# Kernel tuning notes

Hardware: AMD Instinct MI355X
Metric: run time of the kernel (lower is better)

Reference implementation:

```python
import jax, jax.numpy as jnp
import numpy as np

ALPHA = 0.2   # LeakyReLU negative slope (init arg alpha)
H = 256       # hidden_dim
U = 1024      # user pairs -> 2U user nodes
M = 64        # UAV nodes
D = 2 * U     # uniform out-degree per UAV (edges sorted by source)
N = 2 * U + M
E = M * D


def _lstm_dir(x, w_ih, w_hh, b):
    # x: [T, B, I] -> outputs [T, B, Hc]; b = b_ih + b_hh (they only ever add)
    Hc = w_hh.shape[1]
    B = x.shape[1]
    def step(carry, xt):
        h, c = carry
        g = xt @ w_ih.T + h @ w_hh.T + b          # [B, 4*Hc], gate order i,f,g,o
        i, f, gg, o = jnp.split(g, 4, axis=-1)
        c = jax.nn.sigmoid(f) * c + jax.nn.sigmoid(i) * jnp.tanh(gg)
        h = jax.nn.sigmoid(o) * jnp.tanh(c)
        return (h, c), h
    h0 = jnp.zeros((B, Hc), x.dtype)
    _, hs = jax.lax.scan(step, (h0, h0), x)
    return hs


def _bilstm(x, wih, whh, b):
    # wih: [2, 4Hc, I]; whh: [2, 4Hc, Hc]; b: [2, 4Hc]; dir 0 = fwd, 1 = reverse
    fwd = _lstm_dir(x, wih[0], whh[0], b[0])
    rev = _lstm_dir(x[::-1], wih[1], whh[1], b[1])[::-1]
    return jnp.concatenate([fwd, rev], axis=-1)   # [T, B, 2*Hc]


def _mlp2(h, w1, b1, w2, b2):
    h = jax.nn.relu(h @ w1.T + b1)
    return jax.nn.relu(h @ w2.T + b2)


def _forward(x, edge_index, users_num,
             ul_wih, ul_whh, ul_b, uav_lin_w, uav_lin_b,
             msg_w1, msg_b1, msg_w2, msg_b2,
             wq_w, wq_b, wr_w, wr_b, att_w, att_b,
             upd_w1, upd_b1, upd_w2, upd_b2,
             uavl_wih, uavl_whh, uavl_b, lin2_w, lin2_b):
    Un = users_num
    n = x.shape[0]
    m = n - 2 * Un
    # ---- users bidirectional LSTM over the pair (seq_len=2, batch=U) ----
    seq = jnp.stack([x[:Un], x[Un:2 * Un]], axis=0)        # [2, U, 2]
    users = _bilstm(seq, ul_wih, ul_whh, ul_b)             # [2, U, H]
    users = jnp.concatenate([users[0], users[1]], axis=0)  # [2U, H]
    uavs = x[2 * Un:] @ uav_lin_w.T + uav_lin_b            # [M, H]
    h = jnp.concatenate([users, uavs], axis=0)             # [N, H]
    # ---- message passing (flow target_to_source: i=src, aggregate at src) ----
    src, tgt = edge_index[0], edge_index[1]
    xi = h[src]                                            # [E, H]
    xj = h[tgt]                                            # [E, H]
    msg = _mlp2(jnp.concatenate([xi, xj], axis=1), msg_w1, msg_b1, msg_w2, msg_b2)  # [E, H]
    q = xi @ wq_w.T + wq_b
    r = msg @ wr_w.T + wr_b
    a = jax.nn.leaky_relu(jnp.concatenate([q, r], axis=1) @ att_w.T + att_b, ALPHA)  # [E,1]
    # segment softmax: edges sorted by source, uniform degree -> reshape [M, D]
    a = jax.nn.softmax(a.reshape(m, -1), axis=1).reshape(-1, 1)
    # ---- scatter-mean aggregate over source index ----
    agg = jax.ops.segment_sum(a * msg, src, num_segments=n)          # [N, H]
    cnt = jax.ops.segment_sum(jnp.ones((src.shape[0],), x.dtype), src, num_segments=n)
    agg = agg / jnp.maximum(cnt, 1.0)[:, None]
    # ---- update ----
    h2 = _mlp2(jnp.concatenate([agg, h], axis=1), upd_w1, upd_b1, upd_w2, upd_b2)  # [N, H]
    uav_seq = h2[2 * Un:][:, None, :]                      # [M, 1, H]
    uav_out = _bilstm(uav_seq, uavl_wih, uavl_whh, uavl_b)[:, 0, :]  # [M, H]
    out = jnp.concatenate([h2[:2 * Un], uav_out], axis=0)
    return jax.nn.sigmoid(out @ lin2_w.T + lin2_b)         # [N, 2]


def setup_inputs():
    key = jax.random.key(0)
    ks = iter(jax.random.split(key, 32))
    p = lambda *s: jax.random.normal(next(ks), s, jnp.float32) * 0.05
    Hc = H // 2
    x = jax.random.uniform(next(ks), (N, 2), jnp.float32)
    src = jnp.repeat(2 * U + jnp.arange(M), D)
    tgt = jnp.tile(jnp.arange(2 * U), M)
    edge_index = jnp.stack([src, tgt]).astype(jnp.int32)
    return dict(
        x=x, edge_index=edge_index, users_num=U,
        ul_wih=p(2, 4 * Hc, 2), ul_whh=p(2, 4 * Hc, Hc), ul_b=p(2, 4 * Hc),
        uav_lin_w=p(H, 2), uav_lin_b=p(H),
        msg_w1=p(H, 2 * H), msg_b1=p(H), msg_w2=p(H, H), msg_b2=p(H),
        wq_w=p(H, H), wq_b=p(H), wr_w=p(H, H), wr_b=p(H),
        att_w=p(1, 2 * H), att_b=p(1),
        upd_w1=p(H, 2 * H), upd_b1=p(H), upd_w2=p(H, H), upd_b2=p(H),
        uavl_wih=p(2, 4 * Hc, H), uavl_whh=p(2, 4 * Hc, Hc), uavl_b=p(2, 4 * Hc),
        lin2_w=p(2, H), lin2_b=p(2),
    )


def reference(x, edge_index, users_num,
              ul_wih, ul_whh, ul_b, uav_lin_w, uav_lin_b,
              msg_w1, msg_b1, msg_w2, msg_b2,
              wq_w, wq_b, wr_w, wr_b, att_w, att_b,
              upd_w1, upd_b1, upd_w2, upd_b2,
              uavl_wih, uavl_whh, uavl_b, lin2_w, lin2_b):
    return _forward(x, edge_index, users_num,
                    ul_wih, ul_whh, ul_b, uav_lin_w, uav_lin_b,
                    msg_w1, msg_b1, msg_w2, msg_b2,
                    wq_w, wq_b, wr_w, wr_b, att_w, att_b,
                    upd_w1, upd_b1, upd_w2, upd_b2,
                    uavl_wih, uavl_whh, uavl_b, lin2_w, lin2_b)
```

## Files before the change

kernel.cpp:

```cpp
#include <hip/hip_runtime.h>
#include <hip/hip_bf16.h>
#include <hip/hip_fp16.h>
#include <math.h>

#define UQ   1024
#define NUQ  2048
#define MQ   64
#define NN   2112
#define HD   256

typedef __attribute__((ext_vector_type(4))) float f32x4;
typedef __attribute__((ext_vector_type(8))) __bf16 bf16x8;
typedef __attribute__((ext_vector_type(8))) _Float16 f16x8;

#define OFF_HB    0u
#define OFF_HUF   65536u
#define OFF_PUBF  1146880u
#define OFF_PB    2195456u
#define OFF_SPR   2260992u
#define OFF_ATT   2261248u
#define OFF_WHHT  2263552u
#define OFF_WIHT  2787840u
#define OFF_W1F   3836416u
#define OFF_W2F   4098560u
#define OFF_UW1F  4229632u
#define OFF_UW2F  4491776u
#define OFF_CREC  4622848u
#define OFF_H2U   5155328u

__device__ __forceinline__ float sigm(float v) { return 1.f / (1.f + expf(-v)); }

__device__ __forceinline__ int huf_idx(int row, int k) {
  return (((row >> 6) * 8 + (k >> 5)) * 4 + ((row >> 4) & 3)) * 512 +
         (((k >> 3) & 3) * 16 + (row & 15)) * 8 + (k & 7);
}

__device__ __forceinline__ void gl16(const void* g, void* l) {
  __builtin_amdgcn_global_load_lds((const __attribute__((address_space(1))) void*)g,
                                   (__attribute__((address_space(3))) void*)l, 16, 0, 0);
}

__device__ void tile_transpose_perm(const float* __restrict__ in, int in_ld,
                                    float* __restrict__ out, int out_ld,
                                    int k0, int c0) {
  __shared__ float ldt[64][68];
  const int t = threadIdx.x;
  {
    const int ci = t >> 2, kq = t & 3;
    const int c = c0 + ci;
    const int row = (c & 3) * 128 + (c >> 2);
    const float* src = in + row * in_ld + k0 + kq * 16;
#pragma unroll
    for (int e = 0; e < 4; ++e)
      *(f32x4*)&ldt[ci][kq * 16 + e * 4] = *(const f32x4*)(src + e * 4);
  }
  __syncthreads();
  {
    const int kk = t >> 2, cq = t & 3;
    float* dst = out + (k0 + kk) * out_ld + c0 + cq * 16;
#pragma unroll
    for (int e4 = 0; e4 < 4; ++e4) {
      f32x4 v;
#pragma unroll
      for (int j = 0; j < 4; ++j) v[j] = ldt[cq * 16 + e4 * 4 + j][kk];
      *(f32x4*)(dst + e4 * 4) = v;
    }
  }
}

template<int K, typename T>
__device__ void frag_cast16(const float* __restrict__ W, int j0, T* __restrict__ frag) {
  __shared__ float ldc[16][K + 4];
  const int t = threadIdx.x;
  {
    const int jr = t >> 4, kq = t & 15;
    const float* src = W + (j0 + jr) * K + kq * (K / 16);
#pragma unroll
    for (int e = 0; e < K / 64; ++e)
      *(f32x4*)&ldc[jr][kq * (K / 16) + e * 4] = *(const f32x4*)(src + e * 4);
  }
  __syncthreads();
  const int f = j0 >> 4;
  constexpr int nks = K >> 5;
  constexpr int thr_per_ks = 256 / nks;
  constexpr int q_per_thr = 512 / thr_per_ks;
  const int ks = t / thr_per_ks;
  const int q0 = (t % thr_per_ks) * q_per_thr;
#pragma unroll
  for (int h = 0; h < q_per_thr / 8; ++h) {
    T v[8];
#pragma unroll
    for (int e = 0; e < 8; ++e) {
      int q = q0 + h * 8 + e;
      int lane = q >> 3;
      v[e] = (T)ldc[lane & 15][ks * 32 + (lane >> 4) * 8 + (q & 7)];
    }
    *(ulong2*)(frag + (ks * 16 + f) * 512 + q0 + h * 8) = *(ulong2*)v;
  }
}

__global__ __launch_bounds__(256) void k0_prep(
    const float* __restrict__ ul_whh, const float* __restrict__ uavl_wih,
    const float* __restrict__ msg_w1, const float* __restrict__ msg_w2,
    const float* __restrict__ upd_w1, const float* __restrict__ upd_w2,
    const float* __restrict__ att_w,  const float* __restrict__ att_b,
    const float* __restrict__ wq_w,   const float* __restrict__ wq_b,
    const float* __restrict__ wr_w,   const float* __restrict__ wr_b,
    char* __restrict__ ws)
{
  const int b = blockIdx.x, t = threadIdx.x;
  if (b < 32) {
    const int dir = b >> 4, tile = b & 15;
    tile_transpose_perm(ul_whh + dir * 65536, 128,
                        (float*)(ws + OFF_WHHT) + dir * 65536, 512,
                        (tile >> 3) * 64, (tile & 7) * 64);
  } else if (b < 96) {
    const int b2 = b - 32, dir = b2 >> 5, tile = b2 & 31;
    tile_transpose_perm(uavl_wih + dir * 131072, 256,
                        (float*)(ws + OFF_WIHT) + dir * 131072, 512,
                        (tile >> 3) * 64, (tile & 7) * 64);
  } else if (b < 112) {
    frag_cast16<256, _Float16>(msg_w2, (b - 96) * 16, (_Float16*)(ws + OFF_W2F));
  } else if (b < 128) {
    frag_cast16<512, __bf16>(msg_w1, (b - 112) * 16, (__bf16*)(ws + OFF_W1F));
  } else if (b < 144) {
    frag_cast16<512, __bf16>(upd_w1, (b - 128) * 16, (__bf16*)(ws + OFF_UW1F));
  } else if (b < 160) {
    frag_cast16<256, __bf16>(upd_w2, (b - 144) * 16, (__bf16*)(ws + OFF_UW2F));
  } else {
    float* wqa = (float*)(ws + OFF_ATT);
    float* vv  = wqa + 256;
    float* c0  = wqa + 512;
    float sa = 0.f, sr = 0.f;
    for (int j = 0; j < 256; ++j) {
      sa += att_w[j]       * wq_w[j * 256 + t];
      sr += att_w[256 + j] * wr_w[j * 256 + t];
    }
    wqa[t] = sa; vv[t] = sr;
    __shared__ float red[256];
    red[t] = att_w[t] * wq_b[t] + att_w[256 + t] * wr_b[t];
    __syncthreads();
    for (int s = 128; s > 0; s >>= 1) { if (t < s) red[t] += red[t + s]; __syncthreads(); }
    if (t == 0) c0[0] = red[0] + att_b[0];
  }
}

__global__ __launch_bounds__(256) void k1_embed(
    const float* __restrict__ x, const float* __restrict__ ul_wih,
    const float* __restrict__ ul_b, const float* __restrict__ uav_lin_w,
    const float* __restrict__ uav_lin_b, char* __restrict__ ws)
{
  __bf16* huf = (__bf16*)(ws + OFF_HUF);
  const int b = blockIdx.x, tid = threadIdx.x;
  if (b < 256) {
    const float* whhT = (const float*)(ws + OFF_WHHT);
    const int dir = tid >> 7, hc = tid & 127;
    const int u0 = b * 4;
    float wx[4], wy[4], bb[4];
#pragma unroll
    for (int g = 0; g < 4; ++g) {
      int row = g * 128 + hc;
      wx[g] = ul_wih[dir * 1024 + row * 2 + 0];
      wy[g] = ul_wih[dir * 1024 + row * 2 + 1];
      bb[g] = ul_b[dir * 512 + row];
    }
    __shared__ float h1s[2][128][4];
    __shared__ float hout[8][260];
    float c1[4], h1v[4], in1x[4], in1y[4];
#pragma unroll
    for (int uu = 0; uu < 4; ++uu) {
      int u = u0 + uu;
      float ax = x[u * 2], ay = x[u * 2 + 1];
      float bx = x[(UQ + u) * 2], by = x[(UQ + u) * 2 + 1];
      float i0x = dir ? bx : ax, i0y = dir ? by : ay;
      in1x[uu] = dir ? ax : bx; in1y[uu] = dir ? ay : by;
      float gv[4];
#pragma unroll
      for (int g = 0; g < 4; ++g) gv[g] = wx[g] * i0x + wy[g] * i0y + bb[g];
      float ii = sigm(gv[0]), gg = tanhf(gv[2]), oo = sigm(gv[3]);
      c1[uu] = ii * gg;
      h1v[uu] = oo * tanhf(c1[uu]);
      h1s[dir][hc][uu] = h1v[uu];
    }
    __syncthreads();
    float acc[4][4];
#pragma unroll
    for (int uu = 0; uu < 4; ++uu)
#pragma unroll
      for (int g = 0; g < 4; ++g) acc[uu][g] = wx[g] * in1x[uu] + wy[g] * in1y[uu] + bb[g];
#pragma unroll 4
    for (int k = 0; k < 128; ++k) {
      f32x4 hv  = *(const f32x4*)&h1s[dir][k][0];
      f32x4 wv4 = *(const f32x4*)(whhT + dir * 65536 + k * 512 + hc * 4);
#pragma unroll
      for (int uu = 0; uu < 4; ++uu)
#pragma unroll
        for (int g = 0; g < 4; ++g) acc[uu][g] += hv[uu] * wv4[g];
    }
    const int col = dir * 128 + hc;
#pragma unroll
    for (int uu = 0; uu < 4; ++uu) {
      float ii = sigm(acc[uu][0]), ff = sigm(acc[uu][1]);
      float gg = tanhf(acc[uu][2]), oo = sigm(acc[uu][3]);
      float c2 = ff * c1[uu] + ii * gg;
      float h2v = oo * tanhf(c2);
      float va = dir ? h2v : h1v[uu];
      float vb = dir ? h1v[uu] : h2v;
      hout[uu][col] = va;
      hout[4 + uu][col] = vb;
    }
    __syncthreads();
    {
      const int lr = tid >> 5, c = tid & 31;
      bf16x8 v;
#pragma unroll
      for (int e = 0; e < 8; ++e) v[e] = (__bf16)hout[lr][c * 8 + e];
      const int node = (lr < 4) ? (u0 + lr) : (UQ + u0 + lr - 4);
      *(bf16x8*)(huf + huf_idx(node, c * 8)) = v;
    }
  } else {
    float* hb = (float*)(ws + OFF_HB);
    const int j = tid;
    const int mb = (b - 256) * 16;
    for (int m = mb; m < mb + 16; ++m) {
      float xa = x[(NUQ + m) * 2], xb = x[(NUQ + m) * 2 + 1];
      float val = xa * uav_lin_w[j * 2] + xb * uav_lin_w[j * 2 + 1] + uav_lin_b[j];
      hb[m * 256 + j] = val;
      huf[huf_idx(NUQ + m, j)] = (__bf16)val;
    }
  }
}

template<int G, int NKS>
__device__ __forceinline__ void frag_gemm_acc_g(const __bf16* __restrict__ Abase, int g0,
                                                const __bf16* __restrict__ Bbase,
                                                f32x4 acc[G][4]) {
  const int lane = threadIdx.x & 63;
  const int cg = threadIdx.x >> 6;
  for (int ks = 0; ks < NKS; ++ks) {
    bf16x8 Af[G], Bf[4];
#pragma unroll
    for (int g = 0; g < G; ++g)
      Af[g] = *(const bf16x8*)(Abase + ((ks * 4 + g0 + g) * 64 + lane) * 8);
#pragma unroll
    for (int f = 0; f < 4; ++f)
      Bf[f] = *(const bf16x8*)(Bbase + ((ks * 16 + cg * 4 + f) * 64 + lane) * 8);
#pragma unroll
    for (int g = 0; g < G; ++g)
#pragma unroll
      for (int f = 0; f < 4; ++f)
        acc[g][f] = __builtin_amdgcn_mfma_f32_16x16x32_bf16(Af[g], Bf[f], acc[g][f], 0, 0, 0);
  }
}

__global__ __launch_bounds__(256) void k2_proj(const float* __restrict__ msg_b1,
                                               char* __restrict__ ws)
{
  const __bf16* huf = (const __bf16*)(ws + OFF_HUF);
  const __bf16* w1f = (const __bf16*)(ws + OFF_W1F);
  const int b = blockIdx.x;
  const int tid = threadIdx.x;
  const int lane = tid & 63, cg = tid >> 6;
  const int cl = lane & 15, g16 = lane >> 4;
  if (b < 64) {
    f32x4 acc[2][4] = {};
    frag_gemm_acc_g<2, 8>(huf + (b >> 1) * 16384, (b & 1) * 2, w1f + 65536, acc);
    __shared__ float ldt[32][264];
#pragma unroll
    for (int g = 0; g < 2; ++g)
#pragma unroll
      for (int f = 0; f < 4; ++f)
#pragma unroll
        for (int r = 0; r < 4; ++r)
          ldt[g * 16 + g16 * 4 + r][cg * 64 + f * 16 + cl] = acc[g][f][r];
    __syncthreads();
    _Float16* pubf = (_Float16*)(ws + OFF_PUBF);
    const int c2 = b >> 3, r16base = (b & 7) * 2;
#pragma unroll
    for (int p = 0; p < 4; ++p) {
      const int region = p * 4 + (tid >> 6);
      const int ks = region >> 1, r16l = region & 1;
      const int row15 = tid & 15, kg = (tid >> 4) & 3;
      const int row = r16l * 16 + row15;
      f16x8 v;
#pragma unroll
      for (int j = 0; j < 8; ++j) v[j] = (_Float16)ldt[row][ks * 32 + kg * 8 + j];
      const int dst = ((c2 * 8 + ks) * 16 + (r16base + r16l)) * 512 + (kg * 16 + row15) * 8;
      *(f16x8*)(pubf + dst) = v;
    }
  } else if (b == 64) {
    f32x4 acc[4][4] = {};
    frag_gemm_acc_g<4, 8>(huf + 32 * 16384, 0, w1f, acc);
    _Float16* pb = (_Float16*)(ws + OFF_PB);
#pragma unroll
    for (int g = 0; g < 4; ++g)
#pragma unroll
      for (int f = 0; f < 4; ++f)
#pragma unroll
        for (int r = 0; r < 4; ++r) {
          int row = g * 16 + g16 * 4 + r;
          int col = cg * 64 + f * 16 + cl;
          pb[row * 256 + col] = (_Float16)(acc[g][f][r] + msg_b1[col]);
        }
  } else {
    const float* hb  = (const float*)(ws + OFF_HB);
    const float* wqa = (const float*)(ws + OFF_ATT);
    const float* c0  = wqa + 512;
    float* spr = (float*)(ws + OFF_SPR);
    if (tid < 64) {
      float s = 0.f;
      for (int k = 0; k < 256; ++k) s += hb[tid * 256 + k] * wqa[k];
      spr[tid] = s + c0[0];
    }
  }
}

__global__ __launch_bounds__(1024, 2) void k3_edge(const float* __restrict__ msg_b2,
                                                   char* __restrict__ ws)
{
  const char*     PUBF = (const char*)(ws + OFF_PUBF);
  const _Float16* PB   = (const _Float16*)(ws + OFF_PB);
  const float*    spr  = (const float*)(ws + OFF_SPR);
  const float*    vv   = (const float*)(ws + OFF_ATT) + 256;
  const char*     W2F  = (const char*)(ws + OFF_W2F);
  float* crec = (float*)(ws + OFF_CREC);

  __shared__ __align__(16) char bufA[2][16384];
  __shared__ __align__(16) char bufB[2][16384];
  __shared__ float plds[16][64];
  __shared__ float redmax[16], wds[16];
  __shared__ float wvs[4][256];

  const int m = blockIdx.x >> 3, ch = blockIdx.x & 7;
  const int tid = threadIdx.x, wave = tid >> 6, lane = tid & 63;
  const int cl = lane & 15, g16 = lane >> 4;
  const int rg = wave >> 2, cg = wave & 3;
  const int rot = (m + ch) & 7;
  const float sm = spr[m];
  const char* Asrc = PUBF + ch * 131072;
  const _Float16* pbm = PB + m * 256;
  const int bq = ((tid >> 4) & 3) * 8;

  auto repack = [](f16x8 raw, f16x8 pb8) -> f16x8 {
    f16x8 s = raw + pb8;
#pragma unroll
    for (int r = 0; r < 8; ++r) s[r] = s[r] > (_Float16)0 ? s[r] : (_Float16)0;
    return s;
  };

  {
    f16x8 raw = *(const f16x8*)(Asrc + rot * 16384 + tid * 16);
    gl16(W2F + rot * 16384 + tid * 16, &bufB[0][tid * 16]);
    f16x8 pb8 = *(const f16x8*)(pbm + rot * 32 + bq);
    *(f16x8*)(&bufA[0][tid * 16]) = repack(raw, pb8);
  }
  __syncthreads();

  f32x4 acc[4][4] = {};
  for (int i = 0; i < 8; ++i) {
    const int cur = i & 1;
    f16x8 arn{};
    f16x8 pn{};
    if (i < 7) {
      const int ksn = (i + 1 + rot) & 7;
      arn = *(const f16x8*)(Asrc + ksn * 16384 + tid * 16);
      gl16(W2F + ksn * 16384 + tid * 16, &bufB[cur ^ 1][tid * 16]);
      pn = *(const f16x8*)(pbm + ksn * 32 + bq);
    }
    f16x8 Af[4], Bf[4];
#pragma unroll
    for (int g = 0; g < 4; ++g)
      Af[g] = *(const f16x8*)(&bufA[cur][((rg * 4 + g) * 64 + lane) * 16]);
#pragma unroll
    for (int f = 0; f < 4; ++f)
      Bf[f] = *(const f16x8*)(&bufB[cur][((cg * 4 + f) * 64 + lane) * 16]);
    __builtin_amdgcn_s_setprio(1);
#pragma unroll
    for (int g = 0; g < 4; ++g)
#pragma unroll
      for (int f = 0; f < 4; ++f)
        acc[g][f] = __builtin_amdgcn_mfma_f32_16x16x32_f16(Af[g], Bf[f], acc[g][f], 0, 0, 0);
    __builtin_amdgcn_s_setprio(0);
    if (i < 7) {
      *(f16x8*)(&bufA[cur ^ 1][tid * 16]) = repack(arn, pn);
    }
    __syncthreads();
  }

  float p[4][4] = {};
#pragma unroll
  for (int f = 0; f < 4; ++f) {
    const int j = cg * 64 + f * 16 + cl;
    const float b2j = msg_b2[j], vj = vv[j];
#pragma unroll
    for (int g = 0; g < 4; ++g)
#pragma unroll
      for (int r = 0; r < 4; ++r) {
        float mv = fmaxf(acc[g][f][r] + b2j, 0.f);
        acc[g][f][r] = mv;
        p[g][r] += mv * vj;
      }
  }
#pragma unroll
  for (int mask = 1; mask < 16; mask <<= 1)
#pragma unroll
    for (int g = 0; g < 4; ++g)
#pragma unroll
      for (int r = 0; r < 4; ++r) p[g][r] += __shfl_xor(p[g][r], mask);
  if (cl == 0) {
#pragma unroll
    for (int g = 0; g < 4; ++g)
#pragma unroll
      for (int r = 0; r < 4; ++r) plds[wave][g * 16 + g16 * 4 + r] = p[g][r];
  }
  __syncthreads();

  float lr[4][4], wm = -3.4e38f;
#pragma unroll
  for (int g = 0; g < 4; ++g)
#pragma unroll
    for (int r = 0; r < 4; ++r) {
      int row = g * 16 + g16 * 4 + r;
      float l = plds[rg * 4 + 0][row] + plds[rg * 4 + 1][row] +
                plds[rg * 4 + 2][row] + plds[rg * 4 + 3][row] + sm;
      l = l > 0.f ? l : 0.2f * l;
      lr[g][r] = l;
      wm = fmaxf(wm, l);
    }
  wm = fmaxf(wm, __shfl_xor(wm, 16));
  wm = fmaxf(wm, __shfl_xor(wm, 32));
  if (lane == 0) redmax[wave] = wm;
  __syncthreads();
  float Mc = redmax[0];
#pragma unroll
  for (int i = 1; i < 16; ++i) Mc = fmaxf(Mc, redmax[i]);

  float e[4][4], ds = 0.f;
#pragma unroll
  for (int g = 0; g < 4; ++g)
#pragma unroll
    for (int r = 0; r < 4; ++r) { e[g][r] = __expf(lr[g][r] - Mc); ds += e[g][r]; }
  ds += __shfl_xor(ds, 16);
  ds += __shfl_xor(ds, 32);
  if (lane == 0) wds[wave] = ds;

#pragma unroll
  for (int f = 0; f < 4; ++f) {
    float w = 0.f;
#pragma unroll
    for (int g = 0; g < 4; ++g)
#pragma unroll
      for (int r = 0; r < 4; ++r) w += e[g][r] * acc[g][f][r];
    w += __shfl_xor(w, 16);
    w += __shfl_xor(w, 32);
    if (g16 == 0) wvs[rg][cg * 64 + f * 16 + cl] = w;
  }
  __syncthreads();

  float* rec = crec + (m * 8 + ch) * 260;
  if (tid < 256) rec[tid] = wvs[0][tid] + wvs[1][tid] + wvs[2][tid] + wvs[3][tid];
  if (tid == 0) rec[256] = Mc;
  if (tid == 1) rec[257] = wds[0] + wds[4] + wds[8] + wds[12];
}

__global__ __launch_bounds__(256) void k56_update(
    const float* __restrict__ upd_b1, const float* __restrict__ upd_b2,
    const float* __restrict__ lin2_w, const float* __restrict__ lin2_b,
    float* __restrict__ out, char* __restrict__ ws)
{
  const __bf16* huf  = (const __bf16*)(ws + OFF_HUF);
  const __bf16* uw1f = (const __bf16*)(ws + OFF_UW1F);
  const __bf16* uw2f = (const __bf16*)(ws + OFF_UW2F);

  __shared__ __align__(16) __bf16 l1f[8 * 2 * 512];
  __shared__ __align__(16) __bf16 aggf[8 * 2 * 512];
  __shared__ float scs[32][8];
  __shared__ float sS[32];
  __shared__ float l2p[4][32][2];

  const int b = blockIdx.x, tid = threadIdx.x;
  const int lane = tid & 63, cg = tid >> 6;
  const int cl = lane & 15, g16 = lane >> 4;

  f32x4 acc[2][4] = {};
  if (b < 64) {
    frag_gemm_acc_g<2, 8>(huf + (b >> 1) * 16384, (b & 1) * 2, uw1f + 8 * 16 * 512, acc);
  } else {
    const int m0 = (b - 64) * 32;
    const float* crec = (const float*)(ws + OFF_CREC);
    if (tid < 32) {
      const int m = m0 + tid;
      float mx = -3.4e38f;
      for (int c = 0; c < 8; ++c) mx = fmaxf(mx, crec[(m * 8 + c) * 260 + 256]);
      float S = 0.f;
      for (int c = 0; c < 8; ++c) {
        float sc = __expf(crec[(m * 8 + c) * 260 + 256] - mx);
        scs[tid][c] = sc;
        S += sc * crec[(m * 8 + c) * 260 + 257];
      }
      sS[tid] = S;
    }
    __syncthreads();
    for (int ml = 0; ml < 32; ++ml) {
      float A = 0.f;
#pragma unroll
      for (int c = 0; c < 8; ++c) A += scs[ml][c] * crec[((m0 + ml) * 8 + c) * 260 + tid];
      float agg = A / sS[ml] * (1.f / 2048.f);
      aggf[((tid >> 5) * 2 + (ml >> 4)) * 512 + (((tid >> 3) & 3) * 16 + (ml & 15)) * 8 + (tid & 7)] =
          (__bf16)agg;
    }
    __syncthreads();
    const int g0 = (b - 64) * 2;
    const __bf16* hufu = huf + 32 * 16384;
    for (int ks = 0; ks < 8; ++ks) {
      bf16x8 Af[2], Bf[4];
#pragma unroll
      for (int g = 0; g < 2; ++g)
        Af[g] = *(const bf16x8*)(aggf + ((ks * 2 + g) * 64 + lane) * 8);
#pragma unroll
      for (int f = 0; f < 4; ++f)
        Bf[f] = *(const bf16x8*)(uw1f + ((ks * 16 + cg * 4 + f) * 64 + lane) * 8);
#pragma unroll
      for (int g = 0; g < 2; ++g)
#pragma unroll
        for (int f = 0; f < 4; ++f)
          acc[g][f] = __builtin_amdgcn_mfma_f32_16x16x32_bf16(Af[g], Bf[f], acc[g][f], 0, 0, 0);
    }
    for (int ks = 8; ks < 16; ++ks) {
      bf16x8 Af[2], Bf[4];
#pragma unroll
      for (int g = 0; g < 2; ++g)
        Af[g] = *(const bf16x8*)(hufu + (((ks - 8) * 4 + g0 + g) * 64 + lane) * 8);
#pragma unroll
      for (int f = 0; f < 4; ++f)
        Bf[f] = *(const bf16x8*)(uw1f + ((ks * 16 + cg * 4 + f) * 64 + lane) * 8);
#pragma unroll
      for (int g = 0; g < 2; ++g)
#pragma unroll
        for (int f = 0; f < 4; ++f)
          acc[g][f] = __builtin_amdgcn_mfma_f32_16x16x32_bf16(Af[g], Bf[f], acc[g][f], 0, 0, 0);
    }
  }

#pragma unroll
  for (int g = 0; g < 2; ++g)
#pragma unroll
    for (int f = 0; f < 4; ++f) {
      const int col = cg * 64 + f * 16 + cl;
      const float b1 = upd_b1[col];
#pragma unroll
      for (int r = 0; r < 4; ++r) {
        float v = fmaxf(acc[g][f][r] + b1, 0.f);
        l1f[((col >> 5) * 2 + g) * 512 + (((col >> 3) & 3) * 16 + g16 * 4 + r) * 8 + (col & 7)] =
            (__bf16)v;
      }
    }
  __syncthreads();

  f32x4 a2[2][4] = {};
  for (int ks = 0; ks < 8; ++ks) {
    bf16x8 Af[2], Bf[4];
#pragma unroll
    for (int g = 0; g < 2; ++g)
      Af[g] = *(const bf16x8*)(l1f + ((ks * 2 + g) * 64 + lane) * 8);
#pragma unroll
    for (int f = 0; f < 4; ++f)
      Bf[f] = *(const bf16x8*)(uw2f + ((ks * 16 + cg * 4 + f) * 64 + lane) * 8);
#pragma unroll
    for (int g = 0; g < 2; ++g)
#pragma unroll
      for (int f = 0; f < 4; ++f)
        a2[g][f] = __builtin_amdgcn_mfma_f32_16x16x32_bf16(Af[g], Bf[f], a2[g][f], 0, 0, 0);
  }

  if (b < 64) {
    float d0[2][4] = {}, d1[2][4] = {};
#pragma unroll
    for (int f = 0; f < 4; ++f) {
      const int col = cg * 64 + f * 16 + cl;
      const float b2 = upd_b2[col];
      const float w0 = lin2_w[col], w1 = lin2_w[256 + col];
#pragma unroll
      for (int g = 0; g < 2; ++g)
#pragma unroll
        for (int r = 0; r < 4; ++r) {
          float hv = fmaxf(a2[g][f][r] + b2, 0.f);
          d0[g][r] += hv * w0;
          d1[g][r] += hv * w1;
        }
    }
#pragma unroll
    for (int mask = 1; mask < 16; mask <<= 1)
#pragma unroll
      for (int g = 0; g < 2; ++g)
#pragma unroll
        for (int r = 0; r < 4; ++r) {
          d0[g][r] += __shfl_xor(d0[g][r], mask);
          d1[g][r] += __shfl_xor(d1[g][r], mask);
        }
    if (cl == 0) {
#pragma unroll
      for (int g = 0; g < 2; ++g)
#pragma unroll
        for (int r = 0; r < 4; ++r) {
          l2p[cg][g * 16 + g16 * 4 + r][0] = d0[g][r];
          l2p[cg][g * 16 + g16 * 4 + r][1] = d1[g][r];
        }
    }
    __syncthreads();
    if (tid < 32) {
      float s0 = l2p[0][tid][0] + l2p[1][tid][0] + l2p[2][tid][0] + l2p[3][tid][0] + lin2_b[0];
      float s1 = l2p[0][tid][1] + l2p[1][tid][1] + l2p[2][tid][1] + l2p[3][tid][1] + lin2_b[1];
      const int row = b * 32 + tid;
      out[row * 2 + 0] = 1.f / (1.f + expf(-s0));
      out[row * 2 + 1] = 1.f / (1.f + expf(-s1));
    }
  } else {
    float* h2u = (float*)(ws + OFF_H2U);
    const int m0 = (b - 64) * 32;
#pragma unroll
    for (int g = 0; g < 2; ++g)
#pragma unroll
      for (int f = 0; f < 4; ++f) {
        const int col = cg * 64 + f * 16 + cl;
        const float b2 = upd_b2[col];
#pragma unroll
        for (int r = 0; r < 4; ++r) {
          const int rl = g * 16 + g16 * 4 + r;
          h2u[(m0 + rl) * 256 + col] = fmaxf(a2[g][f][r] + b2, 0.f);
        }
      }
  }
}

__global__ __launch_bounds__(1024) void k7_final(
    const float* __restrict__ uavl_b, const float* __restrict__ lin2_w,
    const float* __restrict__ lin2_b, float* __restrict__ out, char* __restrict__ ws)
{
  const float* h2u  = (const float*)(ws + OFF_H2U);
  const float* wihT = (const float*)(ws + OFF_WIHT);
  const int m = blockIdx.x, tid = threadIdx.x;
  __shared__ float xs[256];
  __shared__ f32x4 part[4][256];
  __shared__ float uo[256];
  __shared__ float r0s[4], r1s[4];
  if (tid < 256) xs[tid] = h2u[m * 256 + tid];
  __syncthreads();
  const int kq = tid >> 8, dh = tid & 255;
  const int dir = dh >> 7, hc = dh & 127;
  f32x4 a4 = {0.f, 0.f, 0.f, 0.f};
#pragma unroll 4
  for (int k = 0; k < 64; ++k) {
    float xv = xs[kq * 64 + k];
    f32x4 wv4 = *(const f32x4*)(wihT + dir * 131072 + (kq * 64 + k) * 512 + hc * 4);
#pragma unroll
    for (int g = 0; g < 4; ++g) a4[g] += xv * wv4[g];
  }
  part[kq][dh] = a4;
  __syncthreads();
  if (tid < 256) {
    f32x4 s = part[0][tid];
#pragma unroll
    for (int q = 1; q < 4; ++q) {
      f32x4 p = part[q][tid];
#pragma unroll
      for (int g = 0; g < 4; ++g) s[g] += p[g];
    }
    float bb[4];
#pragma unroll
    for (int g = 0; g < 4; ++g) bb[g] = uavl_b[dir * 512 + g * 128 + hc];
    float ii = sigm(s[0] + bb[0]);
    float gg = tanhf(s[2] + bb[2]);
    float oo = sigm(s[3] + bb[3]);
    uo[dir * 128 + hc] = oo * tanhf(ii * gg);
  }
  __syncthreads();
  if (tid < 256) {
    float p0 = uo[tid] * lin2_w[tid];
    float p1 = uo[tid] * lin2_w[256 + tid];
#pragma unroll
    for (int mask = 1; mask < 64; mask <<= 1) {
      p0 += __shfl_xor(p0, mask);
      p1 += __shfl_xor(p1, mask);
    }
    if ((tid & 63) == 0) { r0s[tid >> 6] = p0; r1s[tid >> 6] = p1; }
  }
  __syncthreads();
  if (tid == 0) {
    float d0 = r0s[0] + r0s[1] + r0s[2] + r0s[3] + lin2_b[0];
    float d1 = r1s[0] + r1s[1] + r1s[2] + r1s[3] + lin2_b[1];
    out[(NUQ + m) * 2 + 0] = 1.f / (1.f + expf(-d0));
    out[(NUQ + m) * 2 + 1] = 1.f / (1.f + expf(-d1));
  }
}

extern "C" void kernel_launch(void* const* d_in, const int* in_sizes, int n_in,
                              void* d_out, int out_size, void* d_ws, size_t ws_size,
                              hipStream_t stream)
{
  const float* x         = (const float*)d_in[0];
  const float* ul_wih    = (const float*)d_in[3];
  const float* ul_whh    = (const float*)d_in[4];
  const float* ul_b      = (const float*)d_in[5];
  const float* uav_lin_w = (const float*)d_in[6];
  const float* uav_lin_b = (const float*)d_in[7];
  const float* msg_w1    = (const float*)d_in[8];
  const float* msg_b1    = (const float*)d_in[9];
  const float* msg_w2    = (const float*)d_in[10];
  const float* msg_b2    = (const float*)d_in[11];
  const float* wq_w      = (const float*)d_in[12];
  const float* wq_b      = (const float*)d_in[13];
  const float* wr_w      = (const float*)d_in[14];
  const float* wr_b      = (const float*)d_in[15];
  const float* att_w     = (const float*)d_in[16];
  const float* att_b     = (const float*)d_in[17];
  const float* upd_w1    = (const float*)d_in[18];
  const float* upd_b1    = (const float*)d_in[19];
  const float* upd_w2    = (const float*)d_in[20];
  const float* upd_b2    = (const float*)d_in[21];
  const float* uavl_wih  = (const float*)d_in[22];
  const float* uavl_b    = (const float*)d_in[24];
  const float* lin2_w    = (const float*)d_in[25];
  const float* lin2_b    = (const float*)d_in[26];
  char* ws = (char*)d_ws;
  float* out = (float*)d_out;

  k0_prep<<<dim3(161), dim3(256), 0, stream>>>(ul_whh, uavl_wih, msg_w1, msg_w2, upd_w1,
                                               upd_w2, att_w, att_b, wq_w, wq_b, wr_w, wr_b, ws);
  k1_embed<<<dim3(260), dim3(256), 0, stream>>>(x, ul_wih, ul_b, uav_lin_w, uav_lin_b, ws);
  k2_proj<<<dim3(66), dim3(256), 0, stream>>>(msg_b1, ws);
  k3_edge<<<dim3(512), dim3(1024), 0, stream>>>(msg_b2, ws);
  k56_update<<<dim3(66), dim3(256), 0, stream>>>(upd_b1, upd_b2, lin2_w, lin2_b, out, ws);
  k7_final<<<dim3(64), dim3(1024), 0, stream>>>(uavl_b, lin2_w, lin2_b, out, ws);
}
```

Baseline: 98.31 us.

## Move UAV LSTM input projection to fp16 MFMA and enlarge user LSTM blocks

The final UAV LSTM gate projection now runs as an fp16 MFMA GEMM over fragment-packed weights and h2u, instead of per-block fp32 FMA loops. h2u is now stored in fp16 fragment layout. The work is split into a 4-block gate kernel and a 64-block reduction kernel, which adds one launch. Separately, the user BiLSTM kernel processes 8 users per block instead of 4 and rotates its k loop start, halving the block count and increasing register reuse of W_hh. The fp16 cast of the weights and h2u adds rounding error.

Result: no change. 99.53 us (+1.2%).

```diff
diff --git a/kernel.cpp b/kernel.cpp
--- a/kernel.cpp
+++ b/kernel.cpp
@@ -20,13 +20,14 @@
 #define OFF_SPR   2260992u
 #define OFF_ATT   2261248u
 #define OFF_WHHT  2263552u
-#define OFF_WIHT  2787840u
 #define OFF_W1F   3836416u
 #define OFF_W2F   4098560u
 #define OFF_UW1F  4229632u
 #define OFF_UW2F  4491776u
 #define OFF_CREC  4622848u
-#define OFF_H2U   5155328u
+#define OFF_WIHF  5155328u
+#define OFF_H2UF  5679616u
+#define OFF_UO    5712384u
 
 __device__ __forceinline__ float sigm(float v) { return 1.f / (1.f + expf(-v)); }
 
@@ -114,19 +115,38 @@
     tile_transpose_perm(ul_whh + dir * 65536, 128,
                         (float*)(ws + OFF_WHHT) + dir * 65536, 512,
                         (tile >> 3) * 64, (tile & 7) * 64);
+  } else if (b < 48) {
+    frag_cast16<256, _Float16>(msg_w2, (b - 32) * 16, (_Float16*)(ws + OFF_W2F));
+  } else if (b < 64) {
+    frag_cast16<512, __bf16>(msg_w1, (b - 48) * 16, (__bf16*)(ws + OFF_W1F));
+  } else if (b < 80) {
+    frag_cast16<512, __bf16>(upd_w1, (b - 64) * 16, (__bf16*)(ws + OFF_UW1F));
   } else if (b < 96) {
-    const int b2 = b - 32, dir = b2 >> 5, tile = b2 & 31;
-    tile_transpose_perm(uavl_wih + dir * 131072, 256,
-                        (float*)(ws + OFF_WIHT) + dir * 131072, 512,
-                        (tile >> 3) * 64, (tile & 7) * 64);
-  } else if (b < 112) {
-    frag_cast16<256, _Float16>(msg_w2, (b - 96) * 16, (_Float16*)(ws + OFF_W2F));
-  } else if (b < 128) {
-    frag_cast16<512, __bf16>(msg_w1, (b - 112) * 16, (__bf16*)(ws + OFF_W1F));
-  } else if (b < 144) {
-    frag_cast16<512, __bf16>(upd_w1, (b - 128) * 16, (__bf16*)(ws + OFF_UW1F));
+    frag_cast16<256, __bf16>(upd_w2, (b - 80) * 16, (__bf16*)(ws + OFF_UW2F));
   } else if (b < 160) {
-    frag_cast16<256, __bf16>(upd_w2, (b - 144) * 16, (__bf16*)(ws + OFF_UW2F));
+    __shared__ float ldc2[16][260];
+    const int b2 = b - 96;
+    {
+      const int jr = t >> 4, kq = t & 15;
+      const int jp = b2 * 16 + jr;
+      const int dir = jp >> 9, rem = jp & 511, hc = rem >> 2, gg = rem & 3;
+      const float* src = uavl_wih + (dir * 512 + gg * 128 + hc) * 256 + kq * 16;
+#pragma unroll
+      for (int e = 0; e < 4; ++e)
+        *(f32x4*)&ldc2[jr][kq * 16 + e * 4] = *(const f32x4*)(src + e * 4);
+    }
+    __syncthreads();
+    _Float16* wf = (_Float16*)(ws + OFF_WIHF);
+    const int ks = t >> 5, sub = t & 31;
+#pragma unroll
+    for (int i = 0; i < 2; ++i) {
+      const int gp = sub * 2 + i;
+      const int cl = gp & 15, g16 = gp >> 4;
+      _Float16 v[8];
+#pragma unroll
+      for (int e = 0; e < 8; ++e) v[e] = (_Float16)ldc2[cl][ks * 32 + g16 * 8 + e];
+      *(ulong2*)(wf + (ks * 64 + b2) * 512 + (g16 * 16 + cl) * 8) = *(ulong2*)v;
+    }
   } else {
     float* wqa = (float*)(ws + OFF_ATT);
     float* vv  = wqa + 256;
@@ -152,10 +172,11 @@
 {
   __bf16* huf = (__bf16*)(ws + OFF_HUF);
   const int b = blockIdx.x, tid = threadIdx.x;
-  if (b < 256) {
+  if (b < 128) {
     const float* whhT = (const float*)(ws + OFF_WHHT);
     const int dir = tid >> 7, hc = tid & 127;
-    const int u0 = b * 4;
+    const int u0 = b * 8;
+    const int rot = b & 127;
     float wx[4], wy[4], bb[4];
 #pragma unroll
     for (int g = 0; g < 4; ++g) {
@@ -164,42 +185,48 @@
       wy[g] = ul_wih[dir * 1024 + row * 2 + 1];
       bb[g] = ul_b[dir * 512 + row];
     }
-    __shared__ float h1s[2][128][4];
-    __shared__ float hout[8][260];
-    float c1[4], h1v[4], in1x[4], in1y[4];
-#pragma unroll
-    for (int uu = 0; uu < 4; ++uu) {
+    __shared__ float h1s[2][128][8];
+    __shared__ float hout[16][264];
+    float c1[8], h1v[8], in1x[8], in1y[8];
+#pragma unroll
+    for (int uu = 0; uu < 8; ++uu) {
       int u = u0 + uu;
       float ax = x[u * 2], ay = x[u * 2 + 1];
       float bx = x[(UQ + u) * 2], by = x[(UQ + u) * 2 + 1];
       float i0x = dir ? bx : ax, i0y = dir ? by : ay;
       in1x[uu] = dir ? ax : bx; in1y[uu] = dir ? ay : by;
-      float gv[4];
-#pragma unroll
-      for (int g = 0; g < 4; ++g) gv[g] = wx[g] * i0x + wy[g] * i0y + bb[g];
-      float ii = sigm(gv[0]), gg = tanhf(gv[2]), oo = sigm(gv[3]);
+      float gv0 = wx[0] * i0x + wy[0] * i0y + bb[0];
+      float gv2 = wx[2] * i0x + wy[2] * i0y + bb[2];
+      float gv3 = wx[3] * i0x + wy[3] * i0y + bb[3];
+      float ii = sigm(gv0), gg = tanhf(gv2), oo = sigm(gv3);
       c1[uu] = ii * gg;
       h1v[uu] = oo * tanhf(c1[uu]);
       h1s[dir][hc][uu] = h1v[uu];
     }
     __syncthreads();
-    float acc[4][4];
-#pragma unroll
-    for (int uu = 0; uu < 4; ++uu)
+    float acc[8][4];
+#pragma unroll
+    for (int uu = 0; uu < 8; ++uu)
 #pragma unroll
       for (int g = 0; g < 4; ++g) acc[uu][g] = wx[g] * in1x[uu] + wy[g] * in1y[uu] + bb[g];
-#pragma unroll 4
-    for (int k = 0; k < 128; ++k) {
-      f32x4 hv  = *(const f32x4*)&h1s[dir][k][0];
+#pragma unroll 2
+    for (int kk = 0; kk < 128; ++kk) {
+      const int k = (kk + rot) & 127;
+      f32x4 hv0 = *(const f32x4*)&h1s[dir][k][0];
+      f32x4 hv1 = *(const f32x4*)&h1s[dir][k][4];
       f32x4 wv4 = *(const f32x4*)(whhT + dir * 65536 + k * 512 + hc * 4);
 #pragma unroll
       for (int uu = 0; uu < 4; ++uu)
 #pragma unroll
-        for (int g = 0; g < 4; ++g) acc[uu][g] += hv[uu] * wv4[g];
+        for (int g = 0; g < 4; ++g) acc[uu][g] += hv0[uu] * wv4[g];
+#pragma unroll
+      for (int uu = 4; uu < 8; ++uu)
+#pragma unroll
+        for (int g = 0; g < 4; ++g) acc[uu][g] += hv1[uu - 4] * wv4[g];
     }
     const int col = dir * 128 + hc;
 #pragma unroll
-    for (int uu = 0; uu < 4; ++uu) {
+    for (int uu = 0; uu < 8; ++uu) {
       float ii = sigm(acc[uu][0]), ff = sigm(acc[uu][1]);
       float gg = tanhf(acc[uu][2]), oo = sigm(acc[uu][3]);
       float c2 = ff * c1[uu] + ii * gg;
@@ -207,21 +234,23 @@
       float va = dir ? h2v : h1v[uu];
       float vb = dir ? h1v[uu] : h2v;
       hout[uu][col] = va;
-      hout[4 + uu][col] = vb;
-    }
-    __syncthreads();
-    {
-      const int lr = tid >> 5, c = tid & 31;
+      hout[8 + uu][col] = vb;
+    }
+    __syncthreads();
+#pragma unroll
+    for (int it = 0; it < 2; ++it) {
+      const int idx = it * 256 + tid;
+      const int lr = idx >> 5, c = idx & 31;
       bf16x8 v;
 #pragma unroll
       for (int e = 0; e < 8; ++e) v[e] = (__bf16)hout[lr][c * 8 + e];
-      const int node = (lr < 4) ? (u0 + lr) : (UQ + u0 + lr - 4);
+      const int node = (lr < 8) ? (u0 + lr) : (UQ + u0 + lr - 8);
       *(bf16x8*)(huf + huf_idx(node, c * 8)) = v;
     }
   } else {
     float* hb = (float*)(ws + OFF_HB);
     const int j = tid;
-    const int mb = (b - 256) * 16;
+    const int mb = (b - 128) * 16;
     for (int m = mb; m < mb + 16; ++m) {
       float xa = x[(NUQ + m) * 2], xb = x[(NUQ + m) * 2 + 1];
       float val = xa * uav_lin_w[j * 2] + xb * uav_lin_w[j * 2 + 1] + uav_lin_b[j];
@@ -616,7 +645,7 @@
       out[row * 2 + 1] = 1.f / (1.f + expf(-s1));
     }
   } else {
-    float* h2u = (float*)(ws + OFF_H2U);
+    _Float16* h2uf = (_Float16*)(ws + OFF_H2UF);
     const int m0 = (b - 64) * 32;
 #pragma unroll
     for (int g = 0; g < 2; ++g)
@@ -626,65 +655,85 @@
         const float b2 = upd_b2[col];
 #pragma unroll
         for (int r = 0; r < 4; ++r) {
-          const int rl = g * 16 + g16 * 4 + r;
-          h2u[(m0 + rl) * 256 + col] = fmaxf(a2[g][f][r] + b2, 0.f);
+          const int row = m0 + g * 16 + g16 * 4 + r;
+          float v = fmaxf(a2[g][f][r] + b2, 0.f);
+          h2uf[((col >> 5) * 4 + (row >> 4)) * 512 +
+               (((col >> 3) & 3) * 16 + (row & 15)) * 8 + (col & 7)] = (_Float16)v;
         }
       }
   }
 }
 
-__global__ __launch_bounds__(1024) void k7_final(
-    const float* __restrict__ uavl_b, const float* __restrict__ lin2_w,
-    const float* __restrict__ lin2_b, float* __restrict__ out, char* __restrict__ ws)
+__global__ __launch_bounds__(256) void k7a_gates(const float* __restrict__ uavl_b,
+                                                 char* __restrict__ ws)
 {
-  const float* h2u  = (const float*)(ws + OFF_H2U);
-  const float* wihT = (const float*)(ws + OFF_WIHT);
+  const _Float16* h2uf = (const _Float16*)(ws + OFF_H2UF);
+  const _Float16* wihf = (const _Float16*)(ws + OFF_WIHF);
+  float* uo = (float*)(ws + OFF_UO);
+  __shared__ float ldt[64][260];
+  const int q = blockIdx.x, tid = threadIdx.x;
+  const int lane = tid & 63, cg = tid >> 6;
+  const int cl = lane & 15, g16 = lane >> 4;
+
+  f32x4 acc[4][4] = {};
+  for (int ks = 0; ks < 8; ++ks) {
+    f16x8 Af[4], Bf[4];
+#pragma unroll
+    for (int g = 0; g < 4; ++g)
+      Af[g] = *(const f16x8*)(h2uf + ((ks * 4 + g) * 64 + lane) * 8);
+#pragma unroll
+    for (int f = 0; f < 4; ++f)
+      Bf[f] = *(const f16x8*)(wihf + ((ks * 64 + q * 16 + cg * 4 + f) * 64 + lane) * 8);
+#pragma unroll
+    for (int g = 0; g < 4; ++g)
+#pragma unroll
+      for (int f = 0; f < 4; ++f)
+        acc[g][f] = __builtin_amdgcn_mfma_f32_16x16x32_f16(Af[g], Bf[f], acc[g][f], 0, 0, 0);
+  }
+
+#pragma unroll
+  for (int f = 0; f < 4; ++f) {
+    const int col = cg * 64 + f * 16 + cl;
+    const int jp = q * 256 + col;
+    const int dir = jp >> 9, rem = jp & 511, hc = rem >> 2, gt = rem & 3;
+    const float bias = uavl_b[dir * 512 + gt * 128 + hc];
+#pragma unroll
+    for (int g = 0; g < 4; ++g)
+#pragma unroll
+      for (int r = 0; r < 4; ++r)
+        ldt[g * 16 + g16 * 4 + r][col] = acc[g][f][r] + bias;
+  }
+  __syncthreads();
+
+  const int dir = q >> 1, hcb = (q & 1) * 64;
+#pragma unroll
+  for (int i = 0; i < 16; ++i) {
+    const int idx = i * 256 + tid;
+    const int m = idx & 63, hcl = idx >> 6;
+    float ii = sigm(ldt[m][hcl * 4 + 0]);
+    float gg = tanhf(ldt[m][hcl * 4 + 2]);
+    float oo = sigm(ldt[m][hcl * 4 + 3]);
+    uo[m * 256 + dir * 128 + hcb + hcl] = oo * tanhf(ii * gg);
+  }
+}
+
+__global__ __launch_bounds__(256) void k7b_final(
+    const float* __restrict__ lin2_w, const float* __restrict__ lin2_b,
+    float* __restrict__ out, char* __restrict__ ws)
+{
+  const float* uo = (const float*)(ws + OFF_UO);
   const int m = blockIdx.x, tid = threadIdx.x;
-  __shared__ float xs[256];
-  __shared__ f32x4 part[4][256];
-  __shared__ float uo[256];
+  float u = uo[m * 256 + tid];
+  float p0 = u * lin2_w[tid];
+  float p1 = u * lin2_w[256 + tid];
+#pragma unroll
+  for (int mask = 1; mask < 64; mask <<= 1) {
+    p0 += __shfl_xor(p0, mask);
+    p1 += __shfl_xor(p1, mask);
+  }
   __shared__ float r0s[4], r1s[4];
-  if (tid < 256) xs[tid] = h2u[m * 256 + tid];
-  __syncthreads();
-  const int kq = tid >> 8, dh = tid & 255;
-  const int dir = dh >> 7, hc = dh & 127;
-  f32x4 a4 = {0.f, 0.f, 0.f, 0.f};
-#pragma unroll 4
-  for (int k = 0; k < 64; ++k) {
-    float xv = xs[kq * 64 + k];
-    f32x4 wv4 = *(const f32x4*)(wihT + dir * 131072 + (kq * 64 + k) * 512 + hc * 4);
-#pragma unroll
-    for (int g = 0; g < 4; ++g) a4[g] += xv * wv4[g];
-  }
-  part[kq][dh] = a4;
-  __syncthreads();
-  if (tid < 256) {
-    f32x4 s = part[0][tid];
-#pragma unroll
-    for (int q = 1; q < 4; ++q) {
-      f32x4 p = part[q][tid];
-#pragma unroll
-      for (int g = 0; g < 4; ++g) s[g] += p[g];
-    }
-    float bb[4];
-#pragma unroll
-    for (int g = 0; g < 4; ++g) bb[g] = uavl_b[dir * 512 + g * 128 + hc];
-    float ii = sigm(s[0] + bb[0]);
-    float gg = tanhf(s[2] + bb[2]);
-    float oo = sigm(s[3] + bb[3]);
-    uo[dir * 128 + hc] = oo * tanhf(ii * gg);
-  }
-  __syncthreads();
-  if (tid < 256) {
-    float p0 = uo[tid] * lin2_w[tid];
-    float p1 = uo[tid] * lin2_w[256 + tid];
-#pragma unroll
-    for (int mask = 1; mask < 64; mask <<= 1) {
-      p0 += __shfl_xor(p0, mask);
-      p1 += __shfl_xor(p1, mask);
-    }
-    if ((tid & 63) == 0) { r0s[tid >> 6] = p0; r1s[tid >> 6] = p1; }
-  }
+  const int lane = tid & 63, wv = tid >> 6;
+  if (lane == 0) { r0s[wv] = p0; r1s[wv] = p1; }
   __syncthreads();
   if (tid == 0) {
     float d0 = r0s[0] + r0s[1] + r0s[2] + r0s[3] + lin2_b[0];
@@ -727,9 +776,10 @@
 
   k0_prep<<<dim3(161), dim3(256), 0, stream>>>(ul_whh, uavl_wih, msg_w1, msg_w2, upd_w1,
                                                upd_w2, att_w, att_b, wq_w, wq_b, wr_w, wr_b, ws);
-  k1_embed<<<dim3(260), dim3(256), 0, stream>>>(x, ul_wih, ul_b, uav_lin_w, uav_lin_b, ws);
+  k1_embed<<<dim3(132), dim3(256), 0, stream>>>(x, ul_wih, ul_b, uav_lin_w, uav_lin_b, ws);
   k2_proj<<<dim3(66), dim3(256), 0, stream>>>(msg_b1, ws);
   k3_edge<<<dim3(512), dim3(1024), 0, stream>>>(msg_b2, ws);
   k56_update<<<dim3(66), dim3(256), 0, stream>>>(upd_b1, upd_b2, lin2_w, lin2_b, out, ws);
-  k7_final<<<dim3(64), dim3(1024), 0, stream>>>(uavl_b, lin2_w, lin2_b, out, ws);
-}
+  k7a_gates<<<dim3(4), dim3(256), 0, stream>>>(uavl_b, ws);
+  k7b_final<<<dim3(64), dim3(256), 0, stream>>>(lin2_w, lin2_b, out, ws);
+}
```
